# Kernel optimization log

Measured on AMD Instinct MI355X. Metric: run time of the kernel, lower is better.

The kernel has to match this reference:

```python
import jax, jax.numpy as jnp
import numpy as np

N_EMBD = 1024
N_HEAD = 16
HEAD_DIM = N_EMBD // N_HEAD
EPS = 1e-5


def setup_inputs() -> dict:
    key = jax.random.key(0)
    ks = jax.random.split(key, 12)
    C = N_EMBD
    s = lambda fan_in: 1.0 / np.sqrt(fan_in)
    return {
        "x": jax.random.normal(ks[0], (2, 2048, C), dtype=jnp.float32),
        "ln1_g": jnp.ones((C,), jnp.float32),
        "ln1_b": jnp.zeros((C,), jnp.float32),
        "w_attn": jax.random.normal(ks[1], (C, 3 * C), jnp.float32) * s(C),
        "b_attn": jnp.zeros((3 * C,), jnp.float32),
        "w_proj": jax.random.normal(ks[2], (C, C), jnp.float32) * s(C),
        "b_proj": jnp.zeros((C,), jnp.float32),
        "ln2_g": jnp.ones((C,), jnp.float32),
        "ln2_b": jnp.zeros((C,), jnp.float32),
        "w_fc": jax.random.normal(ks[3], (C, 4 * C), jnp.float32) * s(C),
        "b_fc": jnp.zeros((4 * C,), jnp.float32),
        "w_fc2": jax.random.normal(ks[4], (4 * C, C), jnp.float32) * s(4 * C),
        "b_fc2": jnp.zeros((C,), jnp.float32),
    }


def _layernorm(x, g, b):
    mu = jnp.mean(x, axis=-1, keepdims=True)
    var = jnp.mean(jnp.square(x - mu), axis=-1, keepdims=True)
    return (x - mu) * jax.lax.rsqrt(var + EPS) * g + b


def _attention(x, w_attn, b_attn, w_proj, b_proj):
    B, T, C = x.shape
    qkv = x @ w_attn + b_attn  # [B,T,3C]
    q, k, v = jnp.split(qkv, 3, axis=-1)
    # [B,H,T,D]
    reshape = lambda t: t.reshape(B, T, N_HEAD, HEAD_DIM).transpose(0, 2, 1, 3)
    q, k, v = reshape(q), reshape(k), reshape(v)
    scale = HEAD_DIM ** (-0.5)
    att = jnp.einsum("bhqd,bhkd->bhqk", q, k) * scale  # [B,H,T,T]
    mask = jnp.tril(jnp.ones((T, T), dtype=bool))
    att = jnp.where(mask, att, -jnp.inf)
    att = jax.nn.softmax(att, axis=-1)
    y = jnp.einsum("bhqk,bhkd->bhqd", att, v)
    y = y.transpose(0, 2, 1, 3).reshape(B, T, C)
    return y @ w_proj + b_proj


def _mlp(x, w_fc, b_fc, w_fc2, b_fc2):
    h = jax.nn.gelu(x @ w_fc + b_fc, approximate=False)  # nn.GELU default = exact erf
    return h @ w_fc2 + b_fc2


def reference(x, ln1_g, ln1_b, w_attn, b_attn, w_proj, b_proj,
              ln2_g, ln2_b, w_fc, b_fc, w_fc2, b_fc2):
    x = x + _attention(_layernorm(x, ln1_g, ln1_b), w_attn, b_attn, w_proj, b_proj)
    x = x + _mlp(_layernorm(x, ln2_g, ln2_b), w_fc, b_fc, w_fc2, b_fc2)
    return x
```

## Files before the change

kernel.cpp:

```cpp
#include <hip/hip_runtime.h>
#include <hip/hip_bf16.h>
#include <math.h>

typedef __attribute__((ext_vector_type(8))) __bf16 bf16x8;
typedef __attribute__((ext_vector_type(4))) float floatx4;
typedef __attribute__((ext_vector_type(8))) unsigned short ushort8;

#define C_EMBD 1024
#define T_SEQ 2048
#define NH 16
#define HD 64

#define WAITV(N) asm volatile("s_waitcnt vmcnt(" #N ")" ::: "memory")
#define WAITL(N) asm volatile("s_waitcnt lgkmcnt(" #N ")" ::: "memory")

static __device__ __forceinline__ unsigned short f2b(float f) {
  __hip_bfloat16 h = __float2bfloat16(f);
  unsigned short u;
  __builtin_memcpy(&u, &h, sizeof(u));
  return u;
}
static __device__ __forceinline__ float b2f(unsigned short u) {
  unsigned int b = ((unsigned int)u) << 16;
  float f;
  __builtin_memcpy(&f, &b, sizeof(f));
  return f;
}

static __device__ __forceinline__ void gload16(const void* g, void* l) {
  __builtin_amdgcn_global_load_lds(
      (__attribute__((address_space(1))) void*)(void*)g,
      (__attribute__((address_space(3))) void*)l, 16, 0, 0);
}

static __device__ __forceinline__ floatx4 mfma_bf16(bf16x8 a, bf16x8 b, floatx4 c) {
  return __builtin_amdgcn_mfma_f32_16x16x32_bf16(a, b, c, 0, 0, 0);
}

__global__ __launch_bounds__(256) void wtrans(const float* __restrict__ in,
                                              unsigned short* __restrict__ out,
                                              int K, int N) {
  __shared__ float t[32][33];
  int n0 = blockIdx.x * 32, k0 = blockIdx.y * 32;
  int tx = threadIdx.x & 31, ty = threadIdx.x >> 5;
#pragma unroll
  for (int i = 0; i < 4; i++)
    t[ty + i * 8][tx] = in[(size_t)(k0 + ty + i * 8) * N + n0 + tx];
  __syncthreads();
#pragma unroll
  for (int i = 0; i < 4; i++)
    out[(size_t)(n0 + ty + i * 8) * K + k0 + tx] = f2b(t[tx][ty + i * 8]);
}

__global__ __launch_bounds__(256) void ln_fwd(const float* __restrict__ x,
                                              const float* __restrict__ g,
                                              const float* __restrict__ bta,
                                              unsigned short* __restrict__ out) {
  int row = blockIdx.x;
  int t = threadIdx.x;
  const float4* xr = (const float4*)(x + (size_t)row * C_EMBD);
  float4 v = xr[t];
  float s = v.x + v.y + v.z + v.w;
  float ss = v.x * v.x + v.y * v.y + v.z * v.z + v.w * v.w;
#pragma unroll
  for (int m = 1; m < 64; m <<= 1) {
    s += __shfl_xor(s, m, 64);
    ss += __shfl_xor(ss, m, 64);
  }
  __shared__ float ps[8];
  int wv = t >> 6;
  if ((t & 63) == 0) { ps[wv] = s; ps[4 + wv] = ss; }
  __syncthreads();
  s = ps[0] + ps[1] + ps[2] + ps[3];
  ss = ps[4] + ps[5] + ps[6] + ps[7];
  float mu = s * (1.0f / C_EMBD);
  float var = ss * (1.0f / C_EMBD) - mu * mu;
  float rs = rsqrtf(var + 1e-5f);
  float4 gv = ((const float4*)g)[t];
  float4 bv = ((const float4*)bta)[t];
  ushort4 o;
  o.x = f2b((v.x - mu) * rs * gv.x + bv.x);
  o.y = f2b((v.y - mu) * rs * gv.y + bv.y);
  o.z = f2b((v.z - mu) * rs * gv.z + bv.z);
  o.w = f2b((v.w - mu) * rs * gv.w + bv.w);
  *(ushort4*)(out + (size_t)row * C_EMBD + t * 4) = o;
}

template <int EP, int MI>
__global__ __launch_bounds__(256) void gemm_bt(const unsigned short* __restrict__ A,
                                               const unsigned short* __restrict__ Bt,
                                               const float* __restrict__ bias,
                                               const float* __restrict__ res,
                                               void* __restrict__ outv,
                                               unsigned short* __restrict__ vt,
                                               int M, int N, int K) {
  __shared__ __align__(16) unsigned short As[MI * 32 * 32];
  __shared__ __align__(16) unsigned short Bs[128 * 32];
  const int tid = threadIdx.x;
  const int wv = tid >> 6, ln = tid & 63;
  const int quad = ln >> 4, l15 = ln & 15;
  const int wm = wv >> 1, wn = wv & 1;
  const int m0 = blockIdx.y * (MI * 32), n0 = blockIdx.x * 128;

  floatx4 acc[MI][4];
#pragma unroll
  for (int i = 0; i < MI; i++)
#pragma unroll
    for (int j = 0; j < 4; j++) acc[i][j] = (floatx4)0.0f;

  const int rowA = ln >> 2;
  const int koff = (ln & 3) * 8;

  for (int k0 = 0; k0 < K; k0 += 32) {
    if (k0) __syncthreads();
#pragma unroll
    for (int hh = 0; hh < MI / 2; ++hh) {
      int r = hh * 64 + wv * 16 + rowA;
      gload16(A + (size_t)(m0 + r) * K + k0 + koff, &As[(hh * 64 + wv * 16) * 32]);
    }
#pragma unroll
    for (int hh = 0; hh < 2; ++hh) {
      int r = hh * 64 + wv * 16 + rowA;
      gload16(Bt + (size_t)(n0 + r) * K + k0 + koff, &Bs[(hh * 64 + wv * 16) * 32]);
    }
    __syncthreads();
    bf16x8 af[MI], bfr[4];
#pragma unroll
    for (int mi = 0; mi < MI; mi++)
      af[mi] = *(const bf16x8*)&As[(wm * (MI * 16) + mi * 16 + l15) * 32 + quad * 8];
#pragma unroll
    for (int ni = 0; ni < 4; ni++)
      bfr[ni] = *(const bf16x8*)&Bs[(wn * 64 + ni * 16 + l15) * 32 + quad * 8];
#pragma unroll
    for (int mi = 0; mi < MI; mi++)
#pragma unroll
      for (int ni = 0; ni < 4; ni++)
        acc[mi][ni] = mfma_bf16(af[mi], bfr[ni], acc[mi][ni]);
  }

#pragma unroll
  for (int mi = 0; mi < MI; mi++) {
#pragma unroll
    for (int ni = 0; ni < 4; ni++) {
      int col = n0 + wn * 64 + ni * 16 + l15;
      int rowb = m0 + wm * (MI * 16) + mi * 16 + quad * 4;
      float bc = bias[col];
      if (EP == 1) {
#pragma unroll
        for (int r = 0; r < 4; r++) {
          size_t idx = (size_t)(rowb + r) * N + col;
          ((float*)outv)[idx] = acc[mi][ni][r] + bc + res[idx];
        }
      }
    }
  }
}

template <int EP>
__global__ __launch_bounds__(512, 2) void gemm256(
    const unsigned short* __restrict__ A, const unsigned short* __restrict__ Bt,
    const float* __restrict__ bias, const float* __restrict__ res,
    void* __restrict__ outv, unsigned short* __restrict__ vt,
    float* __restrict__ p0, float* __restrict__ p12,
    int M, int N, int ldK, int KCH) {
  __shared__ __align__(16) unsigned short As[4][8192];
  __shared__ __align__(16) unsigned short Bs[4][8192];
  const int tid = threadIdx.x;
  const int wv = tid >> 6, ln = tid & 63;
  const int quad = ln >> 4, l15 = ln & 15;
  const int wm = wv >> 2, wn = wv & 3;

  const int gx = gridDim.x;
  const int nwg = gx * gridDim.y;
  int id = blockIdx.y * gx + blockIdx.x;
  const int cpx = nwg >> 3;
  id = (id & 7) * cpx + (id >> 3);
  const int n0 = (id % gx) * 256;
  const int m0 = (id / gx) * 256;
  const int bz = blockIdx.z;

  A += (size_t)bz * KCH;
  Bt += (size_t)bz * KCH;

  const int srowin = ln >> 2;
  const int sqo = ((ln & 3) ^ (ln >> 4)) * 8;
  const unsigned short* aSt = A + (size_t)(m0 + wv * 16 + srowin) * ldK + sqo;
  const unsigned short* bSt = Bt + (size_t)(n0 + wv * 16 + srowin) * ldK + sqo;
  const size_t gstep = (size_t)128 * ldK;

  const int fsw = (quad ^ (l15 >> 2)) * 8;

  floatx4 acc[8][4];
#pragma unroll
  for (int i = 0; i < 8; i++)
#pragma unroll
    for (int j = 0; j < 4; j++) acc[i][j] = (floatx4)0.0f;

  const int NT = KCH >> 5;

  auto stage = [&](int bi, int kt) {
    const unsigned short* aS = aSt + kt * 32;
    const unsigned short* bS = bSt + kt * 32;
#pragma unroll
    for (int g = 0; g < 2; g++) {
      gload16(aS + g * gstep, &As[bi][g * 4096 + wv * 512]);
      gload16(bS + g * gstep, &Bs[bi][g * 4096 + wv * 512]);
    }
  };

  stage(0, 0);
  stage(1, 1);
  stage(2, 2);

  for (int t = 0; t < NT; ++t) {
    const int cur = t & 3;
    if (t + 3 < NT) stage((t + 3) & 3, t + 3);
    const int rem = NT - 1 - t;
    if (rem >= 3) WAITV(12);
    else if (rem == 2) WAITV(8);
    else if (rem == 1) WAITV(4);
    else WAITV(0);
    __builtin_amdgcn_s_barrier();

    const unsigned short* Ac = As[cur];
    const unsigned short* Bc = Bs[cur];
    bf16x8 bF[4], aF0[4], aF1[4];
#pragma unroll
    for (int ni = 0; ni < 4; ni++)
      bF[ni] = *(const bf16x8*)&Bc[(wn * 64 + ni * 16 + l15) * 32 + fsw];
#pragma unroll
    for (int i = 0; i < 4; i++)
      aF0[i] = *(const bf16x8*)&Ac[(wm * 128 + i * 16 + l15) * 32 + fsw];
#pragma unroll
    for (int i = 0; i < 4; i++)
      aF1[i] = *(const bf16x8*)&Ac[(wm * 128 + (4 + i) * 16 + l15) * 32 + fsw];
    WAITL(4);
    __builtin_amdgcn_sched_barrier(0);
    __builtin_amdgcn_s_setprio(1);
#pragma unroll
    for (int mi = 0; mi < 4; mi++)
#pragma unroll
      for (int ni = 0; ni < 4; ni++)
        acc[mi][ni] = mfma_bf16(aF0[mi], bF[ni], acc[mi][ni]);
    __builtin_amdgcn_s_setprio(0);
    __builtin_amdgcn_s_barrier();
    WAITL(0);
    __builtin_amdgcn_sched_barrier(0);
    __builtin_amdgcn_s_setprio(1);
#pragma unroll
    for (int mi = 0; mi < 4; mi++)
#pragma unroll
      for (int ni = 0; ni < 4; ni++)
        acc[4 + mi][ni] = mfma_bf16(aF1[mi], bF[ni], acc[4 + mi][ni]);
    __builtin_amdgcn_s_setprio(0);
    __builtin_amdgcn_s_barrier();
  }

#pragma unroll
  for (int mi = 0; mi < 8; mi++) {
#pragma unroll
    for (int ni = 0; ni < 4; ni++) {
      const int col = n0 + wn * 64 + ni * 16 + l15;
      const int rowb = m0 + wm * 128 + mi * 16 + quad * 4;
      const float bc = bias ? bias[col] : 0.0f;
      if (EP == 1) {
#pragma unroll
        for (int r = 0; r < 4; r++) {
          size_t idx = (size_t)(rowb + r) * N + col;
          ((float*)outv)[idx] = acc[mi][ni][r] + bc + res[idx];
        }
      } else if (EP == 2) {
#pragma unroll
        for (int r = 0; r < 4; r++) {
          float v = acc[mi][ni][r] + bc;
          v = 0.5f * v * (1.0f + erff(v * 0.70710678118f));
          ((unsigned short*)outv)[(size_t)(rowb + r) * N + col] = f2b(v);
        }
      } else if (EP == 3) {
        if (col < 2048) {
#pragma unroll
          for (int r = 0; r < 4; r++)
            ((unsigned short*)outv)[(size_t)(rowb + r) * N + col] =
                f2b(acc[mi][ni][r] + bc);
        } else {
          int dall = col - 2048;
          int hh2 = dall >> 6, dd = dall & 63;
          int bq = rowb >> 11, t0 = rowb & 2047;
          __align__(8) unsigned short pk[4];
#pragma unroll
          for (int r = 0; r < 4; r++) pk[r] = f2b(acc[mi][ni][r] + bc);
          *(ushort4*)&vt[(size_t)((bq * NH + hh2) * HD + dd) * T_SEQ + t0] =
              *(const ushort4*)pk;
        }
      } else {
        if (bz == 3) {
#pragma unroll
          for (int r = 0; r < 4; r++) {
            size_t idx = (size_t)(rowb + r) * N + col;
            ((float*)outv)[idx] = acc[mi][ni][r] + bc + res[idx];
          }
        } else {
          const size_t MN = (size_t)M * N;
          float* pp = (bz == 0) ? p0 : p12 + (size_t)(bz - 1) * MN;
#pragma unroll
          for (int r = 0; r < 4; r++)
            pp[(size_t)(rowb + r) * N + col] = acc[mi][ni][r];
        }
      }
    }
  }
}

__global__ __launch_bounds__(256) void red3(const float* __restrict__ p0,
                                            const float* __restrict__ p12,
                                            float* __restrict__ out) {
  const size_t MN4 = (size_t)4096 * 1024 / 4;
  for (size_t i = (size_t)blockIdx.x * 256 + threadIdx.x; i < MN4;
       i += (size_t)gridDim.x * 256) {
    float4 a = ((const float4*)p0)[i];
    float4 b = ((const float4*)p12)[i];
    float4 c = ((const float4*)p12)[i + MN4];
    float4 o = ((float4*)out)[i];
    o.x += a.x + b.x + c.x;
    o.y += a.y + b.y + c.y;
    o.z += a.z + b.z + c.z;
    o.w += a.w + b.w + c.w;
    ((float4*)out)[i] = o;
  }
}

__global__ __launch_bounds__(256) void attn_fwd(const unsigned short* __restrict__ qkv,
                                                const unsigned short* __restrict__ vt,
                                                unsigned short* __restrict__ y) {
  __shared__ __align__(16) unsigned short Ks[64 * 64];
  __shared__ __align__(16) unsigned short Vs[64 * 64];
  __shared__ __align__(16) unsigned short Ps[4 * 16 * 72];
  const int tid = threadIdx.x;
  const int wv = tid >> 6, ln = tid & 63;
  const int quad = ln >> 4, l15 = ln & 15;
  const int pair = blockIdx.x, h = blockIdx.y, b = blockIdx.z;
  unsigned short* Pw = &Ps[wv * 16 * 72];

  const unsigned short* kbase = qkv + (size_t)b * T_SEQ * 3072 + 1024 + h * HD;
  const unsigned short* vbase = vt + (size_t)(b * NH + h) * HD * T_SEQ;

  int koffs[2], voffs[2], ldst[2];
#pragma unroll
  for (int g = 0; g < 2; g++) {
    int S = wv * 128 + g * 64 + ln;
    int r = S >> 3;
    int c = (S & 7) ^ (r & 7);
    koffs[g] = r * 3072 + c * 8;
    voffs[g] = r * T_SEQ + c * 8;
    ldst[g] = wv * 1024 + g * 512;
  }

  for (int ph = 0; ph < 2; ++ph) {
    const int qt = ph ? (31 - pair) : pair;
    const unsigned short* qp =
        qkv + (size_t)(b * T_SEQ + qt * 64 + wv * 16 + l15) * 3072 + h * HD;
    bf16x8 qf[2];
#pragma unroll
    for (int kc = 0; kc < 2; kc++) {
      ushort8 u = *(const ushort8*)(qp + kc * 32 + quad * 8);
      union { ushort8 u; bf16x8 v; } cv;
#pragma unroll
      for (int j = 0; j < 8; j++) cv.u[j] = f2b(b2f(u[j]) * 0.18033688f);
      qf[kc] = cv.v;
    }

    floatx4 o[4];
#pragma unroll
    for (int dt = 0; dt < 4; dt++) o[dt] = (floatx4)0.0f;
    float lacc = 0.0f;

    auto step = [&](int kt, bool diag) {
      __syncthreads();
#pragma unroll
      for (int g = 0; g < 2; g++) {
        gload16(kbase + (size_t)(kt * 64) * 3072 + koffs[g], &Ks[ldst[g]]);
        gload16(vbase + kt * 64 + voffs[g], &Vs[ldst[g]]);
      }
      __syncthreads();

      floatx4 s[4];
#pragma unroll
      for (int nt = 0; nt < 4; nt++) s[nt] = (floatx4)0.0f;
#pragma unroll
      for (int nt = 0; nt < 4; nt++)
#pragma unroll
        for (int kc = 0; kc < 2; kc++) {
          bf16x8 kf = *(const bf16x8*)
              &Ks[(nt * 16 + l15) * 64 + (((kc * 4 + quad) ^ (l15 & 7)) * 8)];
          s[nt] = mfma_bf16(kf, qf[kc], s[nt]);
        }

      float psum = 0.0f;
#pragma unroll
      for (int nt = 0; nt < 4; nt++) {
        __align__(8) unsigned short pk[4];
#pragma unroll
        for (int r = 0; r < 4; r++) {
          float sv = s[nt][r];
          if (diag && (nt * 16 + quad * 4 + r > wv * 16 + l15)) sv = -1e30f;
          float p = exp2f(sv - 12.0f);
          psum += p;
          pk[r] = f2b(p);
        }
        *(ushort4*)&Pw[l15 * 72 + nt * 16 + quad * 4] = *(const ushort4*)pk;
      }
      lacc += psum;

      bf16x8 pf0 = *(const bf16x8*)&Pw[l15 * 72 + quad * 8];
      bf16x8 pf1 = *(const bf16x8*)&Pw[l15 * 72 + 32 + quad * 8];
#pragma unroll
      for (int dt = 0; dt < 4; dt++) {
        bf16x8 vf0 = *(const bf16x8*)
            &Vs[(dt * 16 + l15) * 64 + ((quad ^ (l15 & 7)) * 8)];
        bf16x8 vf1 = *(const bf16x8*)
            &Vs[(dt * 16 + l15) * 64 + (((4 + quad) ^ (l15 & 7)) * 8)];
        o[dt] = mfma_bf16(vf0, pf0, o[dt]);
        o[dt] = mfma_bf16(vf1, pf1, o[dt]);
      }
    };

    for (int kt = 0; kt < qt; ++kt) step(kt, false);
    step(qt, true);

    lacc += __shfl_xor(lacc, 16, 64);
    lacc += __shfl_xor(lacc, 32, 64);
    float rinv = 1.0f / lacc;
#pragma unroll
    for (int dt = 0; dt < 4; dt++) {
      __align__(8) unsigned short ov[4];
#pragma unroll
      for (int r = 0; r < 4; r++) ov[r] = f2b(o[dt][r] * rinv);
      *(ushort4*)&y[(size_t)(b * T_SEQ + qt * 64 + wv * 16 + l15) * C_EMBD +
                    h * HD + dt * 16 + quad * 4] = *(const ushort4*)ov;
    }
  }
}

extern "C" void kernel_launch(void* const* d_in, const int* in_sizes, int n_in,
                              void* d_out, int out_size, void* d_ws, size_t ws_size,
                              hipStream_t stream) {
  (void)in_sizes; (void)n_in; (void)out_size; (void)ws_size;
  const float* x      = (const float*)d_in[0];
  const float* ln1_g  = (const float*)d_in[1];
  const float* ln1_b  = (const float*)d_in[2];
  const float* w_attn = (const float*)d_in[3];
  const float* b_attn = (const float*)d_in[4];
  const float* w_proj = (const float*)d_in[5];
  const float* b_proj = (const float*)d_in[6];
  const float* ln2_g  = (const float*)d_in[7];
  const float* ln2_b  = (const float*)d_in[8];
  const float* w_fc   = (const float*)d_in[9];
  const float* b_fc   = (const float*)d_in[10];
  const float* w_fc2  = (const float*)d_in[11];
  const float* b_fc2  = (const float*)d_in[12];
  float* out = (float*)d_out;

  char* wsb = (char*)d_ws;
  char* ws = wsb;
  unsigned short* wat  = (unsigned short*)ws; ws += (size_t)3072 * 1024 * 2;
  unsigned short* wpt  = (unsigned short*)ws; ws += (size_t)1024 * 1024 * 2;
  unsigned short* wft  = (unsigned short*)ws; ws += (size_t)4096 * 1024 * 2;
  unsigned short* wf2t = (unsigned short*)ws; ws += (size_t)1024 * 4096 * 2;
  unsigned short* xn   = (unsigned short*)ws; ws += (size_t)4096 * 1024 * 2;
  unsigned short* qkv  = (unsigned short*)ws; ws += (size_t)4096 * 3072 * 2;
  unsigned short* yat  = (unsigned short*)ws; ws += (size_t)4096 * 1024 * 2;
  unsigned short* hbuf = (unsigned short*)ws; ws += (size_t)4096 * 4096 * 2;
  unsigned short* vt = hbuf;
  float* p0  = (float*)wsb;
  float* p12 = (float*)(wsb + (size_t)24 * 1024 * 1024);

  wtrans<<<dim3(3072 / 32, 1024 / 32), 256, 0, stream>>>(w_attn, wat, 1024, 3072);
  wtrans<<<dim3(1024 / 32, 1024 / 32), 256, 0, stream>>>(w_proj, wpt, 1024, 1024);
  wtrans<<<dim3(4096 / 32, 1024 / 32), 256, 0, stream>>>(w_fc, wft, 1024, 4096);
  wtrans<<<dim3(1024 / 32, 4096 / 32), 256, 0, stream>>>(w_fc2, wf2t, 4096, 1024);

  ln_fwd<<<4096, 256, 0, stream>>>(x, ln1_g, ln1_b, xn);
  gemm256<3><<<dim3(3072 / 256, 4096 / 256), 512, 0, stream>>>(
      xn, wat, b_attn, nullptr, qkv, vt, nullptr, nullptr, 4096, 3072, 1024, 1024);
  attn_fwd<<<dim3(16, NH, 2), 256, 0, stream>>>(qkv, vt, yat);
  gemm_bt<1, 2><<<dim3(8, 64), 256, 0, stream>>>(
      yat, wpt, b_proj, x, out, nullptr, 4096, 1024, 1024);
  ln_fwd<<<4096, 256, 0, stream>>>(out, ln2_g, ln2_b, xn);
  gemm256<2><<<dim3(4096 / 256, 4096 / 256), 512, 0, stream>>>(
      xn, wft, b_fc, nullptr, hbuf, nullptr, nullptr, nullptr, 4096, 4096, 1024, 1024);
  gemm256<4><<<dim3(1024 / 256, 4096 / 256, 4), 512, 0, stream>>>(
      hbuf, wf2t, b_fc2, out, out, nullptr, p0, p12, 4096, 1024, 4096, 1024);
  red3<<<2048, 256, 0, stream>>>(p0, p12, out);
}
```

Before: 418.4 us.

## Split GEMM prefetch into halves and triple-buffer attention K/V loads

```diff
diff --git a/kernel.cpp b/kernel.cpp
--- a/kernel.cpp
+++ b/kernel.cpp
@@ -13,6 +13,8 @@
 
 #define WAITV(N) asm volatile("s_waitcnt vmcnt(" #N ")" ::: "memory")
 #define WAITL(N) asm volatile("s_waitcnt lgkmcnt(" #N ")" ::: "memory")
+#define DSR(d, a, OFF) \
+  asm volatile("ds_read_b128 %0, %1 offset:" #OFF : "=v"(d) : "v"(a))
 
 static __device__ __forceinline__ unsigned short f2b(float f) {
   __hip_bfloat16 h = __float2bfloat16(f);
@@ -35,6 +37,10 @@
 
 static __device__ __forceinline__ floatx4 mfma_bf16(bf16x8 a, bf16x8 b, floatx4 c) {
   return __builtin_amdgcn_mfma_f32_16x16x32_bf16(a, b, c, 0, 0, 0);
+}
+
+static __device__ __forceinline__ unsigned int lds_addr(const void* p) {
+  return (unsigned int)(size_t)(__attribute__((address_space(3))) void*)(void*)p;
 }
 
 __global__ __launch_bounds__(256) void wtrans(const float* __restrict__ in,
@@ -156,6 +162,12 @@
   }
 }
 
+#define MFROW(av, m)                               \
+  acc[m][0] = mfma_bf16(av, bF0, acc[m][0]);       \
+  acc[m][1] = mfma_bf16(av, bF1, acc[m][1]);       \
+  acc[m][2] = mfma_bf16(av, bF2, acc[m][2]);       \
+  acc[m][3] = mfma_bf16(av, bF3, acc[m][3]);
+
 template <int EP>
 __global__ __launch_bounds__(512, 2) void gemm256(
     const unsigned short* __restrict__ A, const unsigned short* __restrict__ Bt,
@@ -188,7 +200,11 @@
   const unsigned short* bSt = Bt + (size_t)(n0 + wv * 16 + srowin) * ldK + sqo;
   const size_t gstep = (size_t)128 * ldK;
 
-  const int fsw = (quad ^ (l15 >> 2)) * 8;
+  const int fswb = (quad ^ (l15 >> 2)) * 16;
+  const unsigned int aoff =
+      lds_addr(&As[0][0]) + (unsigned)((wm * 128 + l15) * 64 + fswb);
+  const unsigned int boff =
+      lds_addr(&Bs[0][0]) + (unsigned)((wn * 64 + l15) * 64 + fswb);
 
   floatx4 acc[8][4];
 #pragma unroll
@@ -198,62 +214,46 @@
 
   const int NT = KCH >> 5;
 
-  auto stage = [&](int bi, int kt) {
-    const unsigned short* aS = aSt + kt * 32;
-    const unsigned short* bS = bSt + kt * 32;
-#pragma unroll
-    for (int g = 0; g < 2; g++) {
-      gload16(aS + g * gstep, &As[bi][g * 4096 + wv * 512]);
-      gload16(bS + g * gstep, &Bs[bi][g * 4096 + wv * 512]);
-    }
+  auto stageh = [&](int bi, int kt, int g) {
+    gload16(aSt + kt * 32 + (size_t)g * gstep, &As[bi][g * 4096 + wv * 512]);
+    gload16(bSt + kt * 32 + (size_t)g * gstep, &Bs[bi][g * 4096 + wv * 512]);
   };
 
-  stage(0, 0);
-  stage(1, 1);
-  stage(2, 2);
+  stageh(0, 0, 0); stageh(0, 0, 1);
+  stageh(1, 1, 0); stageh(1, 1, 1);
+  stageh(2, 2, 0); stageh(2, 2, 1);
 
   for (int t = 0; t < NT; ++t) {
     const int cur = t & 3;
-    if (t + 3 < NT) stage((t + 3) & 3, t + 3);
     const int rem = NT - 1 - t;
-    if (rem >= 3) WAITV(12);
-    else if (rem == 2) WAITV(8);
+    if (rem >= 2) WAITV(8);
     else if (rem == 1) WAITV(4);
     else WAITV(0);
     __builtin_amdgcn_s_barrier();
 
-    const unsigned short* Ac = As[cur];
-    const unsigned short* Bc = Bs[cur];
-    bf16x8 bF[4], aF0[4], aF1[4];
-#pragma unroll
-    for (int ni = 0; ni < 4; ni++)
-      bF[ni] = *(const bf16x8*)&Bc[(wn * 64 + ni * 16 + l15) * 32 + fsw];
-#pragma unroll
-    for (int i = 0; i < 4; i++)
-      aF0[i] = *(const bf16x8*)&Ac[(wm * 128 + i * 16 + l15) * 32 + fsw];
-#pragma unroll
-    for (int i = 0; i < 4; i++)
-      aF1[i] = *(const bf16x8*)&Ac[(wm * 128 + (4 + i) * 16 + l15) * 32 + fsw];
-    WAITL(4);
-    __builtin_amdgcn_sched_barrier(0);
-    __builtin_amdgcn_s_setprio(1);
-#pragma unroll
-    for (int mi = 0; mi < 4; mi++)
-#pragma unroll
-      for (int ni = 0; ni < 4; ni++)
-        acc[mi][ni] = mfma_bf16(aF0[mi], bF[ni], acc[mi][ni]);
-    __builtin_amdgcn_s_setprio(0);
+    const unsigned int ab = aoff + (cur << 14);
+    const unsigned int bb = boff + (cur << 14);
+    bf16x8 bF0, bF1, bF2, bF3, aA0, aA1, aA2, aA3;
+    DSR(bF0, bb, 0); DSR(bF1, bb, 1024); DSR(bF2, bb, 2048); DSR(bF3, bb, 3072);
+    DSR(aA0, ab, 0); DSR(aA1, ab, 1024); DSR(aA2, ab, 2048); DSR(aA3, ab, 3072);
+    if (t + 3 < NT) stageh((t + 3) & 3, t + 3, 0);
     __builtin_amdgcn_s_barrier();
     WAITL(0);
     __builtin_amdgcn_sched_barrier(0);
     __builtin_amdgcn_s_setprio(1);
-#pragma unroll
-    for (int mi = 0; mi < 4; mi++)
-#pragma unroll
-      for (int ni = 0; ni < 4; ni++)
-        acc[4 + mi][ni] = mfma_bf16(aF1[mi], bF[ni], acc[4 + mi][ni]);
+    MFROW(aA0, 0) MFROW(aA1, 1) MFROW(aA2, 2) MFROW(aA3, 3)
     __builtin_amdgcn_s_setprio(0);
     __builtin_amdgcn_s_barrier();
+
+    bf16x8 aB0, aB1, aB2, aB3;
+    DSR(aB0, ab, 4096); DSR(aB1, ab, 5120); DSR(aB2, ab, 6144); DSR(aB3, ab, 7168);
+    if (t + 3 < NT) stageh((t + 3) & 3, t + 3, 1);
+    __builtin_amdgcn_s_barrier();
+    WAITL(0);
+    __builtin_amdgcn_sched_barrier(0);
+    __builtin_amdgcn_s_setprio(1);
+    MFROW(aB0, 4) MFROW(aB1, 5) MFROW(aB2, 6) MFROW(aB3, 7)
+    __builtin_amdgcn_s_setprio(0);
   }
 
 #pragma unroll
@@ -332,8 +332,8 @@
 __global__ __launch_bounds__(256) void attn_fwd(const unsigned short* __restrict__ qkv,
                                                 const unsigned short* __restrict__ vt,
                                                 unsigned short* __restrict__ y) {
-  __shared__ __align__(16) unsigned short Ks[64 * 64];
-  __shared__ __align__(16) unsigned short Vs[64 * 64];
+  __shared__ __align__(16) unsigned short Ks[3][64 * 64];
+  __shared__ __align__(16) unsigned short Vs[3][64 * 64];
   __shared__ __align__(16) unsigned short Ps[4 * 16 * 72];
   const int tid = threadIdx.x;
   const int wv = tid >> 6, ln = tid & 63;
@@ -355,6 +355,14 @@
     ldst[g] = wv * 1024 + g * 512;
   }
 
+  auto stage = [&](int kt, int slot) {
+#pragma unroll
+    for (int g = 0; g < 2; g++) {
+      gload16(kbase + (size_t)(kt * 64) * 3072 + koffs[g], &Ks[slot][ldst[g]]);
+      gload16(vbase + kt * 64 + voffs[g], &Vs[slot][ldst[g]]);
+    }
+  };
+
   for (int ph = 0; ph < 2; ++ph) {
     const int qt = ph ? (31 - pair) : pair;
     const unsigned short* qp =
@@ -374,15 +382,18 @@
     for (int dt = 0; dt < 4; dt++) o[dt] = (floatx4)0.0f;
     float lacc = 0.0f;
 
-    auto step = [&](int kt, bool diag) {
-      __syncthreads();
-#pragma unroll
-      for (int g = 0; g < 2; g++) {
-        gload16(kbase + (size_t)(kt * 64) * 3072 + koffs[g], &Ks[ldst[g]]);
-        gload16(vbase + kt * 64 + voffs[g], &Vs[ldst[g]]);
-      }
-      __syncthreads();
-
+    stage(0, 0);
+    if (qt >= 1) stage(1, 1);
+
+    for (int kt = 0; kt <= qt; ++kt) {
+      const int slot = kt % 3;
+      const bool diag = (kt == qt);
+      if (kt < qt) WAITV(4); else WAITV(0);
+      __builtin_amdgcn_s_barrier();
+      if (kt + 2 <= qt) stage(kt + 2, (kt + 2) % 3);
+
+      const unsigned short* Kc = Ks[slot];
+      const unsigned short* Vc = Vs[slot];
       floatx4 s[4];
 #pragma unroll
       for (int nt = 0; nt < 4; nt++) s[nt] = (floatx4)0.0f;
@@ -391,7 +402,7 @@
 #pragma unroll
         for (int kc = 0; kc < 2; kc++) {
           bf16x8 kf = *(const bf16x8*)
-              &Ks[(nt * 16 + l15) * 64 + (((kc * 4 + quad) ^ (l15 & 7)) * 8)];
+              &Kc[(nt * 16 + l15) * 64 + (((kc * 4 + quad) ^ (l15 & 7)) * 8)];
           s[nt] = mfma_bf16(kf, qf[kc], s[nt]);
         }
 
@@ -416,16 +427,13 @@
 #pragma unroll
       for (int dt = 0; dt < 4; dt++) {
         bf16x8 vf0 = *(const bf16x8*)
-            &Vs[(dt * 16 + l15) * 64 + ((quad ^ (l15 & 7)) * 8)];
+            &Vc[(dt * 16 + l15) * 64 + ((quad ^ (l15 & 7)) * 8)];
         bf16x8 vf1 = *(const bf16x8*)
-            &Vs[(dt * 16 + l15) * 64 + (((4 + quad) ^ (l15 & 7)) * 8)];
+            &Vc[(dt * 16 + l15) * 64 + (((4 + quad) ^ (l15 & 7)) * 8)];
         o[dt] = mfma_bf16(vf0, pf0, o[dt]);
         o[dt] = mfma_bf16(vf1, pf1, o[dt]);
       }
-    };
-
-    for (int kt = 0; kt < qt; ++kt) step(kt, false);
-    step(qt, true);
+    }
 
     lacc += __shfl_xor(lacc, 16, 64);
     lacc += __shfl_xor(lacc, 32, 64);
```

After: 389.4 us. -6.9%, faster.
